# Kernel tuning notes

Measured on AMD Instinct MI355X. Metric: run time of the kernel, lower is better.

## Reference

```python
import jax, jax.numpy as jnp
import numpy as np
import math

B, N, H, A, NH = 4, 1024, 1024, 1024, 16
HD = A // NH
MLP_H = int(H * 4.0)          # 4096
FFN = int(MLP_H * 2 / 3)      # 2730 (SwiGLU hidden)
EPS = 1e-6

def _rms(x, w, eps=EPS):
    var = jnp.mean(jnp.square(x), axis=-1, keepdims=True)
    return x * jax.lax.rsqrt(var + eps) * w

def setup_inputs() -> dict:
    key = jax.random.key(0)
    ks = jax.random.split(key, 16)
    def w(k, shape, s=0.02):
        return (jax.random.normal(k, shape) * s).astype(jnp.float32)
    return {
        'x': jax.random.normal(ks[0], (B, N, H), dtype=jnp.float32),
        'c': jax.random.normal(ks[1], (B, H), dtype=jnp.float32),
        'norm1_w': jnp.ones((H,), jnp.float32),
        'compress_w': w(ks[2], (A, H)), 'compress_b': jnp.zeros((A,), jnp.float32),
        'qkv_w': w(ks[3], (3 * A, A)), 'qkv_b': jnp.zeros((3 * A,), jnp.float32),
        'qn_w': jnp.ones((HD,), jnp.float32), 'kn_w': jnp.ones((HD,), jnp.float32),
        'proj_w': w(ks[4], (A, A)), 'proj_b': jnp.zeros((A,), jnp.float32),
        'expand_w': w(ks[5], (H, A)), 'expand_b': jnp.zeros((H,), jnp.float32),
        'norm2_w': jnp.ones((H,), jnp.float32),
        'w12_w': w(ks[6], (2 * FFN, H)), 'w12_b': jnp.zeros((2 * FFN,), jnp.float32),
        'w3_w': w(ks[7], (H, FFN)), 'w3_b': jnp.zeros((H,), jnp.float32),
        'ada_w': w(ks[8], (6 * H, H)), 'ada_b': jnp.zeros((6 * H,), jnp.float32),
    }

def reference(x, c, norm1_w, compress_w, compress_b, qkv_w, qkv_b, qn_w, kn_w,
              proj_w, proj_b, expand_w, expand_b, norm2_w, w12_w, w12_b,
              w3_w, w3_b, ada_w, ada_b):
    # adaLN: SiLU -> Linear -> chunk 6
    ada = jax.nn.silu(c) @ ada_w.T + ada_b                      # [B, 6H]
    sh_msa, sc_msa, g_msa, sh_mlp, sc_mlp, g_mlp = jnp.split(ada, 6, axis=-1)

    def modulate(h, shift, scale):
        return h * (1 + scale[:, None, :]) + shift[:, None, :]

    # --- compact attention branch ---
    h = modulate(_rms(x, norm1_w), sh_msa, sc_msa)              # [B,N,H]
    hc = h @ compress_w.T + compress_b                          # [B,N,A]
    qkv = (hc @ qkv_w.T + qkv_b).reshape(B, N, 3, NH, HD)
    qkv = jnp.transpose(qkv, (2, 0, 3, 1, 4))                   # [3,B,NH,N,HD]
    q, k, v = qkv[0], qkv[1], qkv[2]
    q = _rms(q, qn_w)
    k = _rms(k, kn_w)
    scale = 1.0 / math.sqrt(HD)
    # manual fp32 softmax attention (dropout_p=0 -> identity)
    aw = jnp.einsum('bhnd,bhmd->bhnm', q.astype(jnp.float32),
                    k.astype(jnp.float32)) * scale              # [B,NH,N,N]
    aw = jax.nn.softmax(aw, axis=-1)
    o = jnp.einsum('bhnm,bhmd->bhnd', aw, v)                    # [B,NH,N,HD]
    o = jnp.transpose(o, (0, 2, 1, 3)).reshape(B, N, A)
    o = o @ proj_w.T + proj_b                                   # [B,N,A]
    o = o @ expand_w.T + expand_b                               # [B,N,H]
    x = x + g_msa[:, None, :] * o

    # --- SwiGLU FFN branch ---
    h2 = modulate(_rms(x, norm2_w), sh_mlp, sc_mlp)
    x12 = h2 @ w12_w.T + w12_b                                  # [B,N,2*FFN]
    x1, x2 = jnp.split(x12, 2, axis=-1)
    hid = jax.nn.silu(x1) * x2
    x = x + g_mlp[:, None, :] * (hid @ w3_w.T + w3_b)
    return x
```

## Files before the change

kernel.cpp:

```cpp
#include <hip/hip_runtime.h>
#include <hip/hip_bf16.h>
#include <cstdint>
#include <cstddef>

typedef unsigned short u16;
typedef __bf16 bf16x8 __attribute__((ext_vector_type(8)));
typedef __bf16 bf16x4 __attribute__((ext_vector_type(4)));
typedef short   s16x4 __attribute__((ext_vector_type(4)));
typedef float    f32x4 __attribute__((ext_vector_type(4)));
typedef unsigned short u16x2 __attribute__((ext_vector_type(2)));
typedef unsigned short u16x4 __attribute__((ext_vector_type(4)));
typedef unsigned short u16x8 __attribute__((ext_vector_type(8)));

#define DEVI static __device__ __forceinline__

DEVI float b2f(u16 u){ union{unsigned i; float v;} x; x.i=((unsigned)u)<<16; return x.v; }
DEVI u16 f2b(float f){ union{float v; unsigned i;} x; x.v=f; unsigned r=x.i+0x7FFFu+((x.i>>16)&1u); return (u16)(r>>16); }
DEVI f32x4 mfma16(bf16x8 a, bf16x8 b, f32x4 c){ return __builtin_amdgcn_mfma_f32_16x16x32_bf16(a,b,c,0,0,0); }
DEVI f32x4 mfma16k16(bf16x4 a, bf16x4 b, f32x4 c){
#if __has_builtin(__builtin_amdgcn_mfma_f32_16x16x16_bf16)
  return __builtin_amdgcn_mfma_f32_16x16x16_bf16(a,b,c,0,0,0);
#elif __has_builtin(__builtin_amdgcn_mfma_f32_16x16x16bf16_1k)
  return __builtin_amdgcn_mfma_f32_16x16x16bf16_1k((s16x4)a,(s16x4)b,c,0,0,0);
#else
  asm volatile("v_mfma_f32_16x16x16_bf16 %0, %1, %2, %0" : "+v"(c) : "v"(a), "v"(b));
  return c;
#endif
}
DEVI float fexp2(float x){ return __builtin_amdgcn_exp2f(x); }
DEVI void gload16(const void* g, void* l){
  __builtin_amdgcn_global_load_lds((const __attribute__((address_space(1))) void*)g,
                                   (__attribute__((address_space(3))) void*)l, 16, 0, 0);
}
DEVI float silu_f(float x){ return x/(1.f+__expf(-x)); }

static constexpr size_t OFF_WC   = 0;
static constexpr size_t OFF_WQKV = OFF_WC   + (size_t)1024*1024*2;
static constexpr size_t OFF_WPROJ= OFF_WQKV + (size_t)3072*1024*2;
static constexpr size_t OFF_WEXP = OFF_WPROJ+ (size_t)1024*1024*2;
static constexpr size_t OFF_WW12 = OFF_WEXP + (size_t)1024*1024*2;
static constexpr size_t OFF_WW3  = OFF_WW12 + (size_t)5632*1024*2;
static constexpr size_t OFF_ADA  = OFF_WW3  + (size_t)1024*2752*2;
static constexpr size_t OFF_X2   = OFF_ADA  + (size_t)4*6144*4;
static constexpr size_t OFF_P1   = OFF_X2   + (size_t)4096*1024*4;
static constexpr size_t OFF_H1   = OFF_P1;
static constexpr size_t OFF_HC   = OFF_H1   + (size_t)4096*1024*2;
static constexpr size_t OFF_QKVO = OFF_HC   + (size_t)4096*1024*2;
static constexpr size_t OFF_X12  = OFF_P1;
static constexpr size_t OFF_P2   = OFF_P1   + (size_t)4096*5632*2;
static constexpr size_t OFF_Q    = OFF_P2;
static constexpr size_t OFF_K    = OFF_Q    + (size_t)64*1024*64*2;
static constexpr size_t OFF_VT   = OFF_K    + (size_t)64*1024*64*2;
static constexpr size_t OFF_O    = OFF_VT   + (size_t)64*1024*64*2;
static constexpr size_t OFF_PR   = OFF_O    + (size_t)4096*1024*2;
static constexpr size_t OFF_H2   = OFF_PR   + (size_t)4096*1024*2;
static constexpr size_t OFF_HID  = OFF_P2;

__global__ __launch_bounds__(256) void convert_pad(const float* __restrict__ src, u16* __restrict__ dst,
                                                   int R, int C, int Cpad)
{
  int r = blockIdx.y;
  int c0 = (blockIdx.x*256 + threadIdx.x)*4;
  if (c0 >= Cpad) return;
  u16x4 o;
#pragma unroll
  for (int j=0;j<4;j++){
    int cc = c0+j;
    float f = (r < R && cc < C) ? src[(size_t)r*C + cc] : 0.f;
    o[j] = f2b(f);
  }
  *(u16x4*)&dst[(size_t)r*Cpad + c0] = o;
}

__global__ __launch_bounds__(256) void ada_kernel(const float* __restrict__ c,
    const float* __restrict__ aw, const float* __restrict__ ab, float* __restrict__ ada)
{
  __shared__ float s[4][1024];
  int t = threadIdx.x;
#pragma unroll
  for (int i=0;i<16;i++){
    int idx = i*256 + t;
    float cv = c[idx];
    s[idx>>10][idx&1023] = cv/(1.f+__expf(-cv));
  }
  __syncthreads();
  int wid = t>>6, lane = t&63;
  int j = blockIdx.x*4 + wid;
  const f32x4* wp = (const f32x4*)(aw + (size_t)j*1024);
  float a0=0,a1=0,a2=0,a3=0;
#pragma unroll
  for (int i=0;i<4;i++){
    f32x4 wv = wp[i*64 + lane];
    int k0 = (i*64+lane)*4;
#pragma unroll
    for (int e=0;e<4;e++){
      float w = wv[e];
      a0 += w*s[0][k0+e]; a1 += w*s[1][k0+e]; a2 += w*s[2][k0+e]; a3 += w*s[3][k0+e];
    }
  }
#pragma unroll
  for (int mask=1; mask<64; mask<<=1){
    a0 += __shfl_xor(a0, mask); a1 += __shfl_xor(a1, mask);
    a2 += __shfl_xor(a2, mask); a3 += __shfl_xor(a3, mask);
  }
  if (lane==0){
    float bv = ab[j];
    ada[0*6144 + j] = a0 + bv;
    ada[1*6144 + j] = a1 + bv;
    ada[2*6144 + j] = a2 + bv;
    ada[3*6144 + j] = a3 + bv;
  }
}

__global__ __launch_bounds__(256) void rms_mod(const float* __restrict__ x,
    const float* __restrict__ w, const float* __restrict__ ada, int chunkSh,
    u16* __restrict__ out)
{
  int row = blockIdx.x;
  int b = row>>10;
  int t = threadIdx.x;
  int wid = t>>6, lane = t&63;
  f32x4 v = *(const f32x4*)(x + (size_t)row*1024 + t*4);
  float ss = v[0]*v[0]+v[1]*v[1]+v[2]*v[2]+v[3]*v[3];
#pragma unroll
  for (int mask=1; mask<64; mask<<=1) ss += __shfl_xor(ss, mask);
  __shared__ float red[4];
  if (lane==0) red[wid]=ss;
  __syncthreads();
  float rinv = rsqrtf((red[0]+red[1]+red[2]+red[3])*(1.f/1024.f) + 1e-6f);
  int cc = t*4;
  const float* shp = ada + (size_t)b*6144 + (size_t)chunkSh*1024 + cc;
  u16x4 o;
#pragma unroll
  for (int jj=0;jj<4;jj++){
    float val = v[jj]*rinv*w[cc+jj];
    val = val*(1.f+shp[jj+1024]) + shp[jj];
    o[jj] = f2b(val);
  }
  *(u16x4*)&out[(size_t)row*1024 + cc] = o;
}

template<int EPI>
__global__ __launch_bounds__(256) void gemm_dr(
    const u16* __restrict__ A, const u16* __restrict__ Bw, const float* __restrict__ bias,
    int N, int K, int nbias, u16* __restrict__ outb,
    const float* __restrict__ xres, const float* __restrict__ ada, int adaChunk,
    float* __restrict__ outf)
{
  constexpr int RU = 8192;
  __shared__ __align__(16) u16 lds[6*RU];
  int t = threadIdx.x;
  int lane = t&63, w = t>>6;
  int wr = (w>>1)*64, wc = (w&1)*64;
  int lr = lane&15, lg = lane>>4;
  int id = blockIdx.y*8 + blockIdx.x;
  int xcd = id&7, loc = id>>3;
  int bm = xcd*4 + (loc>>3);
  int bn = loc&7;
  int srow = t>>2;
  int schunk = ((t&3) ^ (srow&3))*8;
  const u16* pA = A  + (size_t)(bm*128 + srow)*K + schunk;
  const u16* pB = Bw + (size_t)(bn*128 + srow)*K + schunk;
  int rp = (lg ^ (lr&3))*8;
  int aoff = (wr + lr)*32 + rp;
  int boff = 4096 + (wc + lr)*32 + rp;
  f32x4 acc[4][4] = {};
  int NT = K>>5;

  auto stage = [&](int kt, int slot){
    u16* dst = &lds[slot*RU];
    const u16* sa = pA + (size_t)kt*32;
    const u16* sb = pB + (size_t)kt*32;
    gload16(sa,                dst + t*8);
    gload16(sa + (size_t)64*K, dst + 2048 + t*8);
    gload16(sb,                dst + 4096 + t*8);
    gload16(sb + (size_t)64*K, dst + 6144 + t*8);
  };
  auto compute = [&](int slot){
    const u16* lb = &lds[slot*RU];
    bf16x8 af[4], bfr[4];
#pragma unroll
    for (int m=0;m<4;m++) af[m]  = *(const bf16x8*)&lb[aoff + m*512];
#pragma unroll
    for (int n=0;n<4;n++) bfr[n] = *(const bf16x8*)&lb[boff + n*512];
    __builtin_amdgcn_s_setprio(1);
#pragma unroll
    for (int m=0;m<4;m++)
#pragma unroll
      for (int n=0;n<4;n++)
        acc[m][n] = mfma16(af[m], bfr[n], acc[m][n]);
    __builtin_amdgcn_s_setprio(0);
  };

#pragma unroll
  for (int i=0;i<5;i++) stage(i, i);
  asm volatile("s_waitcnt vmcnt(16)" ::: "memory");
  __builtin_amdgcn_s_barrier();
  __builtin_amdgcn_sched_barrier(0);

  int cur = 0, stg = 5;
  for (int kt=0; kt<NT-5; ++kt){
    stage(kt+5, stg);
    compute(cur);
    asm volatile("s_waitcnt vmcnt(16)" ::: "memory");
    __builtin_amdgcn_s_barrier();
    __builtin_amdgcn_sched_barrier(0);
    cur = (cur==5)?0:cur+1;
    stg = (stg==5)?0:stg+1;
  }
  compute(cur); cur=(cur==5)?0:cur+1;
  asm volatile("s_waitcnt vmcnt(12)" ::: "memory");
  __builtin_amdgcn_s_barrier(); __builtin_amdgcn_sched_barrier(0);
  compute(cur); cur=(cur==5)?0:cur+1;
  asm volatile("s_waitcnt vmcnt(8)" ::: "memory");
  __builtin_amdgcn_s_barrier(); __builtin_amdgcn_sched_barrier(0);
  compute(cur); cur=(cur==5)?0:cur+1;
  asm volatile("s_waitcnt vmcnt(4)" ::: "memory");
  __builtin_amdgcn_s_barrier(); __builtin_amdgcn_sched_barrier(0);
  compute(cur); cur=(cur==5)?0:cur+1;
  asm volatile("s_waitcnt vmcnt(0)" ::: "memory");
  __builtin_amdgcn_s_barrier(); __builtin_amdgcn_sched_barrier(0);
  compute(cur);

#pragma unroll
  for (int n=0;n<4;n++){
    int col = bn*128 + wc + n*16 + lr;
    float bv = (col < nbias) ? bias[col] : 0.f;
#pragma unroll
    for (int m=0;m<4;m++){
      int row0 = bm*128 + wr + m*16 + lg*4;
#pragma unroll
      for (int r=0;r<4;r++){
        int row = row0 + r;
        float v = acc[m][n][r] + bv;
        if constexpr (EPI==0){
          outb[(size_t)row*N + col] = f2b(v);
        } else {
          int bb = row>>10;
          float g = ada[(size_t)bb*6144 + (size_t)adaChunk*1024 + col];
          outf[(size_t)row*1024 + col] = xres[(size_t)row*1024 + col] + g*v;
        }
      }
    }
  }
}

__global__ __launch_bounds__(256,2) void gemm_dp2(
    const u16* __restrict__ A, const u16* __restrict__ Bw, const float* __restrict__ bias,
    int N, int K, int nbias, u16* __restrict__ outb)
{
  constexpr int AU = 128*32;
  constexpr int RU = AU + 256*32;
  __shared__ __align__(16) u16 lds[3*RU];
  int t = threadIdx.x;
  int lane = t&63, w = t>>6;
  int wr = w>>1, wc = w&1;
  int lr = lane&15, lg = lane>>4;
  int bm = blockIdx.y, bn = blockIdx.x;
  int schunk = ((t&3) ^ ((t>>3)&3))*8;
  const u16* pA = A  + (size_t)(bm*128 + (t>>2))*K + schunk;
  const u16* pB = Bw + (size_t)(bn*256 + (t>>2))*K + schunk;
  int rsw  = (lg ^ ((lr>>1)&3))*8;
  int aoff = (wr*64 + lr)*32 + rsw;
  int boff = AU + (wc*128 + lr)*32 + rsw;
  f32x4 acc[4][8] = {};
  int NT = K>>5;

  auto stage = [&](int kt, int rg){
    u16* dst = &lds[rg*RU];
    const u16* sa = pA + (size_t)kt*32;
    const u16* sb = pB + (size_t)kt*32;
    gload16(sa,                  dst + t*8);
    gload16(sa + (size_t)64*K,   dst + 2048 + t*8);
#pragma unroll
    for (int i=0;i<4;i++)
      gload16(sb + (size_t)(i*64)*K, dst + AU + i*2048 + t*8);
  };

  stage(0, 0);
  stage(1, 1);
  asm volatile("s_waitcnt vmcnt(6)" ::: "memory");
  __builtin_amdgcn_s_barrier();
  __builtin_amdgcn_sched_barrier(0);

  int cur = 0, stg = 2;
  for (int kt=0; kt<NT; ++kt){
    const u16* lb = &lds[cur*RU];
    if (kt+2 < NT) stage(kt+2, stg);
    bf16x8 af[4], bfr[8];
#pragma unroll
    for (int mf=0;mf<4;mf++) af[mf] = *(const bf16x8*)&lb[aoff + mf*512];
#pragma unroll
    for (int nf=0;nf<8;nf++) bfr[nf] = *(const bf16x8*)&lb[boff + nf*512];
    __builtin_amdgcn_s_setprio(1);
#pragma unroll
    for (int mf=0;mf<4;mf++)
#pragma unroll
      for (int nf=0;nf<8;nf++)
        acc[mf][nf] = mfma16(af[mf], bfr[nf], acc[mf][nf]);
    __builtin_amdgcn_s_setprio(0);
    if (kt+2 < NT){
      asm volatile("s_waitcnt vmcnt(6)" ::: "memory");
    } else if (kt+1 < NT){
      asm volatile("s_waitcnt vmcnt(0)" ::: "memory");
    }
    if (kt+1 < NT){
      __builtin_amdgcn_s_barrier();
      __builtin_amdgcn_sched_barrier(0);
    }
    cur = (cur==2)?0:cur+1;
    stg = (stg==2)?0:stg+1;
  }
#pragma unroll
  for (int nf=0;nf<8;nf++){
    int col = bn*256 + wc*128 + nf*16 + lr;
    float bv = (col < nbias) ? bias[col] : 0.f;
#pragma unroll
    for (int mf=0; mf<4; mf++){
      int row0 = bm*128 + wr*64 + mf*16 + lg*4;
#pragma unroll
      for (int r=0;r<4;r++)
        outb[(size_t)(row0+r)*N + col] = f2b(acc[mf][nf][r] + bv);
    }
  }
}

__global__ __launch_bounds__(256) void repack_qkv(const u16* __restrict__ qkvO,
    const float* __restrict__ qnw, const float* __restrict__ knw,
    u16* __restrict__ qO, u16* __restrict__ kO, u16* __restrict__ vO)
{
  __shared__ u16 ldsv[64][64];
  int bh = blockIdx.y, b = bh>>4, h = bh&15;
  int n0 = blockIdx.x*64;
  int t = threadIdx.x;
  int nr = t>>2, qd = (t&3)*16;
  const u16* rowp = qkvO + (size_t)(b*1024 + n0 + nr)*3072;
  {
    u16x8 a0 = *(const u16x8*)(rowp + h*64 + qd);
    u16x8 a1 = *(const u16x8*)(rowp + h*64 + qd + 8);
    float f[16]; float ss=0;
#pragma unroll
    for (int jj=0;jj<8;jj++){ f[jj]=b2f(a0[jj]); f[8+jj]=b2f(a1[jj]); }
#pragma unroll
    for (int jj=0;jj<16;jj++) ss += f[jj]*f[jj];
    ss += __shfl_xor(ss,1); ss += __shfl_xor(ss,2);
    float rinv = rsqrtf(ss*(1.f/64.f)+1e-6f)*0.125f*1.44269504089f;
    u16x8 o0,o1;
#pragma unroll
    for (int jj=0;jj<8;jj++){ o0[jj]=f2b(f[jj]*rinv*qnw[qd+jj]); o1[jj]=f2b(f[8+jj]*rinv*qnw[qd+8+jj]); }
    u16* dst = qO + ((size_t)bh*1024 + n0 + nr)*64 + qd;
    *(u16x8*)dst = o0; *(u16x8*)(dst+8) = o1;
  }
  {
    u16x8 a0 = *(const u16x8*)(rowp + 1024 + h*64 + qd);
    u16x8 a1 = *(const u16x8*)(rowp + 1024 + h*64 + qd + 8);
    float f[16]; float ss=0;
#pragma unroll
    for (int jj=0;jj<8;jj++){ f[jj]=b2f(a0[jj]); f[8+jj]=b2f(a1[jj]); }
#pragma unroll
    for (int jj=0;jj<16;jj++) ss += f[jj]*f[jj];
    ss += __shfl_xor(ss,1); ss += __shfl_xor(ss,2);
    float rinv = rsqrtf(ss*(1.f/64.f)+1e-6f);
    u16x8 o0,o1;
#pragma unroll
    for (int jj=0;jj<8;jj++){ o0[jj]=f2b(f[jj]*rinv*knw[qd+jj]); o1[jj]=f2b(f[8+jj]*rinv*knw[qd+8+jj]); }
    int t16 = (n0 + nr)>>4, lrk = nr&15;
    {
      int d0 = qd, c = d0>>5, lg = (d0>>3)&3;
      *(u16x8*)(kO + (size_t)bh*65536 + ((size_t)(t16*2+c)*64 + lg*16 + lrk)*8) = o0;
    }
    {
      int d0 = qd+8, c = d0>>5, lg = (d0>>3)&3;
      *(u16x8*)(kO + (size_t)bh*65536 + ((size_t)(t16*2+c)*64 + lg*16 + lrk)*8) = o1;
    }
  }
  {
    u16x8 a0 = *(const u16x8*)(rowp + 2048 + h*64 + qd);
    u16x8 a1 = *(const u16x8*)(rowp + 2048 + h*64 + qd + 8);
#pragma unroll
    for (int jj=0;jj<8;jj++){ ldsv[qd+jj][nr] = a0[jj]; ldsv[qd+8+jj][nr] = a1[jj]; }
  }
  __syncthreads();
  {
    int d = t>>2, ns = (t&3)*16;
    int tt = d>>4, lrv = d&15;
    int m = (n0 + ns)>>5;
    int hf = (ns>>4)&1;
    u16* basep = vO + (size_t)bh*65536 + ((size_t)(m*4+tt)*64 + lrv)*8 + hf*4;
#pragma unroll
    for (int g=0; g<4; ++g){
      u16x4 wv4 = { ldsv[d][ns+g*4], ldsv[d][ns+g*4+1], ldsv[d][ns+g*4+2], ldsv[d][ns+g*4+3] };
      *(u16x4*)(basep + (size_t)g*128) = wv4;
    }
  }
}

__global__ __launch_bounds__(512) void attn_fwd(const u16* __restrict__ qO,
    const u16* __restrict__ kO, const u16* __restrict__ vO, u16* __restrict__ o)
{
  __shared__ __align__(16) float obuf[4][64][16];
  __shared__ __align__(16) float mlb[4][2][2][16];
  int bh = blockIdx.y, b = bh>>4, h = bh&15;
  int w = threadIdx.x>>6, lane = threadIdx.x&63;
  int pair = w>>1, half = w&1;
  int lr = lane&15, lg = lane>>4;
  int q0 = blockIdx.x*64 + pair*16;
  const u16* qp = qO + ((size_t)bh*1024 + q0 + lr)*64 + lg*8;
  bf16x8 qf0 = *(const bf16x8*)qp;
  bf16x8 qf1 = *(const bf16x8*)(qp + 32);
  const u16* kb = kO + (size_t)bh*65536 + (size_t)half*32768 + (size_t)lane*8;
  const u16* vb = vO + (size_t)bh*65536 + (size_t)half*32768 + (size_t)lane*8;
  f32x4 oacc[4] = {};
  float mrun = -3.0e38f, lrun = 0.f;
  for (int it=0; it<16; ++it){
    const u16* kp = kb + (size_t)it*4096;
    bf16x8 k00 = *(const bf16x8*)(kp);
    bf16x8 k01 = *(const bf16x8*)(kp + 512);
    bf16x8 k10 = *(const bf16x8*)(kp + 1024);
    bf16x8 k11 = *(const bf16x8*)(kp + 1536);
    f32x4 s0 = {}, s1 = {};
    s0 = mfma16(k00, qf0, s0); s0 = mfma16(k01, qf1, s0);
    s1 = mfma16(k10, qf0, s1); s1 = mfma16(k11, qf1, s1);
    const u16* vp = vb + (size_t)it*2048;
    bf16x8 vv[4];
#pragma unroll
    for (int tt=0;tt<4;tt++) vv[tt] = *(const bf16x8*)(vp + tt*512);
    float pm = fmaxf(fmaxf(fmaxf(s0[0],s0[1]),fmaxf(s0[2],s0[3])),
                     fmaxf(fmaxf(s1[0],s1[1]),fmaxf(s1[2],s1[3])));
    pm = fmaxf(pm, __shfl_xor(pm, 16));
    pm = fmaxf(pm, __shfl_xor(pm, 32));
    if (__any(pm > mrun + 8.f)){
      float mnew = fmaxf(mrun, pm);
      float alpha = fexp2(mrun - mnew);
      mrun = mnew;
      lrun *= alpha;
      float ar[4];
#pragma unroll
      for (int r=0;r<4;r++) ar[r] = __shfl(alpha, lg*4 + r);
#pragma unroll
      for (int tt=0;tt<4;tt++)
#pragma unroll
        for (int r=0;r<4;r++) oacc[tt][r] *= ar[r];
    }
    float p0[4], p1[4]; float ls = 0.f;
#pragma unroll
    for (int r=0;r<4;r++){ p0[r]=fexp2(s0[r]-mrun); p1[r]=fexp2(s1[r]-mrun); ls += p0[r]+p1[r]; }
    ls += __shfl_xor(ls, 16); ls += __shfl_xor(ls, 32);
    lrun += ls;
    bf16x4 pa0, pa1;
#pragma unroll
    for (int r=0;r<4;r++){ pa0[r] = (__bf16)p0[r]; pa1[r] = (__bf16)p1[r]; }
#pragma unroll
    for (int tt=0;tt<4;tt++){
      bf16x4* vh = (bf16x4*)&vv[tt];
      oacc[tt] = mfma16k16(pa0, vh[0], oacc[tt]);
      oacc[tt] = mfma16k16(pa1, vh[1], oacc[tt]);
    }
  }
  if (lg==0){ mlb[pair][half][0][lr] = mrun; mlb[pair][half][1][lr] = lrun; }
  __syncthreads();
  f32x4 m0 = *(const f32x4*)&mlb[pair][0][0][lg*4];
  f32x4 l0 = *(const f32x4*)&mlb[pair][0][1][lg*4];
  f32x4 m1 = *(const f32x4*)&mlb[pair][1][0][lg*4];
  f32x4 l1 = *(const f32x4*)&mlb[pair][1][1][lg*4];
  f32x4 fh;
#pragma unroll
  for (int r=0;r<4;r++){
    float m = fmaxf(m0[r], m1[r]);
    float e0 = fexp2(m0[r]-m), e1 = fexp2(m1[r]-m);
    float li = 1.f/(l0[r]*e0 + l1[r]*e1);
    fh[r] = (half ? e1 : e0)*li;
  }
  if (half==1){
#pragma unroll
    for (int tt=0;tt<4;tt++){
      f32x4 tv;
#pragma unroll
      for (int r=0;r<4;r++) tv[r] = oacc[tt][r]*fh[r];
      *(f32x4*)&obuf[pair][lane][tt*4] = tv;
    }
  }
  __syncthreads();
  if (half==0){
#pragma unroll
    for (int tt=0;tt<4;tt++){
      f32x4 p = *(const f32x4*)&obuf[pair][lane][tt*4];
#pragma unroll
      for (int r=0;r<4;r++){
        int row = (b<<10) + q0 + lg*4 + r;
        int col = h*64 + tt*16 + lr;
        o[(size_t)row*1024 + col] = f2b(oacc[tt][r]*fh[r] + p[r]);
      }
    }
  }
}

__global__ __launch_bounds__(256) void swiglu_k(const u16* __restrict__ x12, u16* __restrict__ hid)
{
  int r = blockIdx.y;
  int c4 = blockIdx.x*256 + threadIdx.x;
  if (c4 >= 688) return;
  int cc = c4*4;
  const u16* rowp = x12 + (size_t)r*5632;
  u16x4 x1 = *(const u16x4*)(rowp + cc);
  u16x2 x2a = *(const u16x2*)(rowp + 2730 + cc);
  u16x2 x2b = *(const u16x2*)(rowp + 2730 + cc + 2);
  u16 x2v[4] = {x2a[0],x2a[1],x2b[0],x2b[1]};
  u16x4 o;
#pragma unroll
  for (int jj=0;jj<4;jj++){
    float a = b2f(x1[jj]);
    float g = silu_f(a)*b2f(x2v[jj]);
    o[jj] = (cc+jj < 2730) ? f2b(g) : (u16)0;
  }
  *(u16x4*)&hid[(size_t)r*2752 + cc] = o;
}

extern "C" void kernel_launch(void* const* d_in, const int* in_sizes, int n_in,
                              void* d_out, int out_size, void* d_ws, size_t ws_size,
                              hipStream_t stream)
{
  (void)in_sizes; (void)n_in; (void)out_size; (void)ws_size;
  const float* x    = (const float*)d_in[0];
  const float* c    = (const float*)d_in[1];
  const float* n1w  = (const float*)d_in[2];
  const float* cw   = (const float*)d_in[3];
  const float* cb   = (const float*)d_in[4];
  const float* qkvw = (const float*)d_in[5];
  const float* qkvb = (const float*)d_in[6];
  const float* qnw  = (const float*)d_in[7];
  const float* knw  = (const float*)d_in[8];
  const float* pw   = (const float*)d_in[9];
  const float* pb   = (const float*)d_in[10];
  const float* ew   = (const float*)d_in[11];
  const float* eb   = (const float*)d_in[12];
  const float* n2w  = (const float*)d_in[13];
  const float* w12w = (const float*)d_in[14];
  const float* w12b = (const float*)d_in[15];
  const float* w3w  = (const float*)d_in[16];
  const float* w3b  = (const float*)d_in[17];
  const float* adaw = (const float*)d_in[18];
  const float* adab = (const float*)d_in[19];
  float* out = (float*)d_out;
  char* ws = (char*)d_ws;
  auto U = [&](size_t off){ return (u16*)(ws + off); };
  auto F = [&](size_t off){ return (float*)(ws + off); };

  convert_pad<<<dim3(1,1024), 256, 0, stream>>>(cw,   U(OFF_WC),   1024, 1024, 1024);
  convert_pad<<<dim3(1,3072), 256, 0, stream>>>(qkvw, U(OFF_WQKV), 3072, 1024, 1024);
  convert_pad<<<dim3(1,1024), 256, 0, stream>>>(pw,   U(OFF_WPROJ),1024, 1024, 1024);
  convert_pad<<<dim3(1,1024), 256, 0, stream>>>(ew,   U(OFF_WEXP), 1024, 1024, 1024);
  convert_pad<<<dim3(1,5632), 256, 0, stream>>>(w12w, U(OFF_WW12), 5460, 1024, 1024);
  convert_pad<<<dim3(3,1024), 256, 0, stream>>>(w3w,  U(OFF_WW3),  1024, 2730, 2752);

  ada_kernel<<<1536, 256, 0, stream>>>(c, adaw, adab, F(OFF_ADA));

  rms_mod<<<4096, 256, 0, stream>>>(x, n1w, F(OFF_ADA), 0, U(OFF_H1));
  gemm_dr<0><<<dim3(8,32), 256, 0, stream>>>(U(OFF_H1), U(OFF_WC), cb, 1024, 1024, 1024, U(OFF_HC), nullptr, nullptr, 0, nullptr);
  gemm_dp2<<<dim3(12,32), 256, 0, stream>>>(U(OFF_HC), U(OFF_WQKV), qkvb, 3072, 1024, 3072, U(OFF_QKVO));
  repack_qkv<<<dim3(16,64), 256, 0, stream>>>(U(OFF_QKVO), qnw, knw, U(OFF_Q), U(OFF_K), U(OFF_VT));
  attn_fwd<<<dim3(16,64), 512, 0, stream>>>(U(OFF_Q), U(OFF_K), U(OFF_VT), U(OFF_O));
  gemm_dr<0><<<dim3(8,32), 256, 0, stream>>>(U(OFF_O), U(OFF_WPROJ), pb, 1024, 1024, 1024, U(OFF_PR), nullptr, nullptr, 0, nullptr);
  gemm_dr<1><<<dim3(8,32), 256, 0, stream>>>(U(OFF_PR), U(OFF_WEXP), eb, 1024, 1024, 1024, nullptr, x, F(OFF_ADA), 2, F(OFF_X2));

  rms_mod<<<4096, 256, 0, stream>>>(F(OFF_X2), n2w, F(OFF_ADA), 3, U(OFF_H2));
  gemm_dp2<<<dim3(22,32), 256, 0, stream>>>(U(OFF_H2), U(OFF_WW12), w12b, 5632, 1024, 5460, U(OFF_X12));
  swiglu_k<<<dim3(3,4096), 256, 0, stream>>>(U(OFF_X12), U(OFF_HID));
  gemm_dr<1><<<dim3(8,32), 256, 0, stream>>>(U(OFF_HID), U(OFF_WW3), w3b, 1024, 2752, 1024, nullptr, F(OFF_X2), F(OFF_ADA), 5, out);
}
```

Before: 309.6 us.

## Fuse SwiGLU into W12 GEMM epilogue via interleaved weight rows

The W12 weights are converted into an interleaved layout: each group of 16 rows holds 8 x1 rows followed by the 8 matching x2 rows. A new epilogue in the dual-pass GEMM pairs x1 and x2 accumulators across lanes with a shuffle and writes silu(x1)*x2 straight into the hidden buffer. This drops the separate SwiGLU kernel and the full bf16 round-trip of the 5632-wide intermediate. The LDS swizzle pattern in gemm_dr is also changed. The padded hidden columns are no longer explicitly zeroed, so correctness relies on the zero-padded W3 columns.

```diff
diff --git a/kernel.cpp b/kernel.cpp
--- a/kernel.cpp
+++ b/kernel.cpp
@@ -46,7 +46,6 @@
 static constexpr size_t OFF_H1   = OFF_P1;
 static constexpr size_t OFF_HC   = OFF_H1   + (size_t)4096*1024*2;
 static constexpr size_t OFF_QKVO = OFF_HC   + (size_t)4096*1024*2;
-static constexpr size_t OFF_X12  = OFF_P1;
 static constexpr size_t OFF_P2   = OFF_P1   + (size_t)4096*5632*2;
 static constexpr size_t OFF_Q    = OFF_P2;
 static constexpr size_t OFF_K    = OFF_Q    + (size_t)64*1024*64*2;
@@ -70,6 +69,23 @@
     o[j] = f2b(f);
   }
   *(u16x4*)&dst[(size_t)r*Cpad + c0] = o;
+}
+
+__global__ __launch_bounds__(256) void convert_w12i(const float* __restrict__ src, u16* __restrict__ dst)
+{
+  int rp = blockIdx.y;
+  int c0 = threadIdx.x*4;
+  int g = rp>>4, w = rp&15;
+  int sr = g*8 + (w&7);
+  bool valid = sr < 2730;
+  int srow = (w<8) ? sr : 2730 + sr;
+  u16x4 o;
+#pragma unroll
+  for (int j=0;j<4;j++){
+    float f = valid ? src[(size_t)srow*1024 + c0 + j] : 0.f;
+    o[j] = f2b(f);
+  }
+  *(u16x4*)&dst[(size_t)rp*1024 + c0] = o;
 }
 
 __global__ __launch_bounds__(256) void ada_kernel(const float* __restrict__ c,
@@ -158,10 +174,10 @@
   int bm = xcd*4 + (loc>>3);
   int bn = loc&7;
   int srow = t>>2;
-  int schunk = ((t&3) ^ (srow&3))*8;
+  int schunk = ((t&3) ^ ((t>>3)&3))*8;
   const u16* pA = A  + (size_t)(bm*128 + srow)*K + schunk;
   const u16* pB = Bw + (size_t)(bn*128 + srow)*K + schunk;
-  int rp = (lg ^ (lr&3))*8;
+  int rp = (lg ^ ((lr>>1)&3))*8;
   int aoff = (wr + lr)*32 + rp;
   int boff = 4096 + (wc + lr)*32 + rp;
   f32x4 acc[4][4] = {};
@@ -245,6 +261,7 @@
   }
 }
 
+template<int EPI>
 __global__ __launch_bounds__(256,2) void gemm_dp2(
     const u16* __restrict__ A, const u16* __restrict__ Bw, const float* __restrict__ bias,
     int N, int K, int nbias, u16* __restrict__ outb)
@@ -311,16 +328,41 @@
     cur = (cur==2)?0:cur+1;
     stg = (stg==2)?0:stg+1;
   }
-#pragma unroll
-  for (int nf=0;nf<8;nf++){
-    int col = bn*256 + wc*128 + nf*16 + lr;
-    float bv = (col < nbias) ? bias[col] : 0.f;
-#pragma unroll
-    for (int mf=0; mf<4; mf++){
-      int row0 = bm*128 + wr*64 + mf*16 + lg*4;
-#pragma unroll
-      for (int r=0;r<4;r++)
-        outb[(size_t)(row0+r)*N + col] = f2b(acc[mf][nf][r] + bv);
+  if constexpr (EPI==0){
+#pragma unroll
+    for (int nf=0;nf<8;nf++){
+      int col = bn*256 + wc*128 + nf*16 + lr;
+      float bv = (col < nbias) ? bias[col] : 0.f;
+#pragma unroll
+      for (int mf=0; mf<4; mf++){
+        int row0 = bm*128 + wr*64 + mf*16 + lg*4;
+#pragma unroll
+        for (int r=0;r<4;r++)
+          outb[(size_t)(row0+r)*N + col] = f2b(acc[mf][nf][r] + bv);
+      }
+    }
+  } else {
+    bool x1lane = (lr&8)==0;
+#pragma unroll
+    for (int nf=0;nf<8;nf++){
+      int P = bn*128 + (wc*8+nf)*8 + (lr&7);
+      bool vP = (P < 2730);
+      float bv = vP ? bias[x1lane ? P : 2730+P] : 0.f;
+#pragma unroll
+      for (int mf=0; mf<4; mf++){
+        int row0 = bm*128 + wr*64 + mf*16 + lg*4;
+#pragma unroll
+        for (int r=0;r<4;r++){
+          float v = acc[mf][nf][r] + bv;
+          float pv = __shfl_xor(v, 8);
+          float x1 = x1lane ? v : pv;
+          float x2 = x1lane ? pv : v;
+          if (x1lane && vP){
+            float gv = silu_f(x1)*x2;
+            outb[(size_t)(row0+r)*2752 + P] = f2b(gv);
+          }
+        }
+      }
     }
   }
 }
@@ -495,27 +537,6 @@
   }
 }
 
-__global__ __launch_bounds__(256) void swiglu_k(const u16* __restrict__ x12, u16* __restrict__ hid)
-{
-  int r = blockIdx.y;
-  int c4 = blockIdx.x*256 + threadIdx.x;
-  if (c4 >= 688) return;
-  int cc = c4*4;
-  const u16* rowp = x12 + (size_t)r*5632;
-  u16x4 x1 = *(const u16x4*)(rowp + cc);
-  u16x2 x2a = *(const u16x2*)(rowp + 2730 + cc);
-  u16x2 x2b = *(const u16x2*)(rowp + 2730 + cc + 2);
-  u16 x2v[4] = {x2a[0],x2a[1],x2b[0],x2b[1]};
-  u16x4 o;
-#pragma unroll
-  for (int jj=0;jj<4;jj++){
-    float a = b2f(x1[jj]);
-    float g = silu_f(a)*b2f(x2v[jj]);
-    o[jj] = (cc+jj < 2730) ? f2b(g) : (u16)0;
-  }
-  *(u16x4*)&hid[(size_t)r*2752 + cc] = o;
-}
-
 extern "C" void kernel_launch(void* const* d_in, const int* in_sizes, int n_in,
                               void* d_out, int out_size, void* d_ws, size_t ws_size,
                               hipStream_t stream)
@@ -550,21 +571,20 @@
   convert_pad<<<dim3(1,3072), 256, 0, stream>>>(qkvw, U(OFF_WQKV), 3072, 1024, 1024);
   convert_pad<<<dim3(1,1024), 256, 0, stream>>>(pw,   U(OFF_WPROJ),1024, 1024, 1024);
   convert_pad<<<dim3(1,1024), 256, 0, stream>>>(ew,   U(OFF_WEXP), 1024, 1024, 1024);
-  convert_pad<<<dim3(1,5632), 256, 0, stream>>>(w12w, U(OFF_WW12), 5460, 1024, 1024);
+  convert_w12i<<<dim3(1,5632), 256, 0, stream>>>(w12w, U(OFF_WW12));
   convert_pad<<<dim3(3,1024), 256, 0, stream>>>(w3w,  U(OFF_WW3),  1024, 2730, 2752);
 
   ada_kernel<<<1536, 256, 0, stream>>>(c, adaw, adab, F(OFF_ADA));
 
   rms_mod<<<4096, 256, 0, stream>>>(x, n1w, F(OFF_ADA), 0, U(OFF_H1));
   gemm_dr<0><<<dim3(8,32), 256, 0, stream>>>(U(OFF_H1), U(OFF_WC), cb, 1024, 1024, 1024, U(OFF_HC), nullptr, nullptr, 0, nullptr);
-  gemm_dp2<<<dim3(12,32), 256, 0, stream>>>(U(OFF_HC), U(OFF_WQKV), qkvb, 3072, 1024, 3072, U(OFF_QKVO));
+  gemm_dp2<0><<<dim3(12,32), 256, 0, stream>>>(U(OFF_HC), U(OFF_WQKV), qkvb, 3072, 1024, 3072, U(OFF_QKVO));
   repack_qkv<<<dim3(16,64), 256, 0, stream>>>(U(OFF_QKVO), qnw, knw, U(OFF_Q), U(OFF_K), U(OFF_VT));
   attn_fwd<<<dim3(16,64), 512, 0, stream>>>(U(OFF_Q), U(OFF_K), U(OFF_VT), U(OFF_O));
   gemm_dr<0><<<dim3(8,32), 256, 0, stream>>>(U(OFF_O), U(OFF_WPROJ), pb, 1024, 1024, 1024, U(OFF_PR), nullptr, nullptr, 0, nullptr);
   gemm_dr<1><<<dim3(8,32), 256, 0, stream>>>(U(OFF_PR), U(OFF_WEXP), eb, 1024, 1024, 1024, nullptr, x, F(OFF_ADA), 2, F(OFF_X2));
 
   rms_mod<<<4096, 256, 0, stream>>>(F(OFF_X2), n2w, F(OFF_ADA), 3, U(OFF_H2));
-  gemm_dp2<<<dim3(22,32), 256, 0, stream>>>(U(OFF_H2), U(OFF_WW12), w12b, 5632, 1024, 5460, U(OFF_X12));
-  swiglu_k<<<dim3(3,4096), 256, 0, stream>>>(U(OFF_X12), U(OFF_HID));
+  gemm_dp2<2><<<dim3(22,32), 256, 0, stream>>>(U(OFF_H2), U(OFF_WW12), w12b, 5632, 1024, 5460, U(OFF_HID));
   gemm_dr<1><<<dim3(8,32), 256, 0, stream>>>(U(OFF_HID), U(OFF_WW3), w3b, 1024, 2752, 1024, nullptr, F(OFF_X2), F(OFF_ADA), 5, out);
 }
```

Result: no change. 305.9 us (-1.2%).
